# Performance work log

Measured on AMD Instinct MI355X. Metric: run time of the kernel, lower is better.

The kernel has to match this reference:

```python
import jax, jax.numpy as jnp
import numpy as np
import math

B, D, OUT = 512, 128, 100000
S, M = 32.0, 0.5
COS_M, SIN_M = math.cos(M), math.sin(M)
TH = math.cos(math.pi - M)
MM = math.sin(math.pi - M) * M
M1 = M2 = M3 = M5 = 1.0


def setup_inputs() -> dict:
    key = jax.random.key(0)
    k1, k2, k3, k4, k5, k6 = jax.random.split(key, 6)
    x = jax.random.normal(k1, (B, D), dtype=jnp.float32)
    label = jax.random.randint(k2, (B,), 0, OUT)
    k = jax.random.uniform(k3, (1, 1, 1024, 1024), dtype=jnp.float32)
    x0 = jax.random.uniform(k4, (1, 3, 112, 96), dtype=jnp.float32)
    img = jax.random.uniform(k5, (1, 3, 112, 96), dtype=jnp.float32)
    # xavier_uniform for [OUT, D]
    limit = math.sqrt(6.0 / (OUT + D))
    W = jax.random.uniform(k6, (OUT, D), minval=-limit, maxval=limit, dtype=jnp.float32)
    return {"x": x, "label": label, "k": k, "x0": x0, "img": img, "W": W}


def _arcmargin(x, W, label):
    xn = x / jnp.linalg.norm(x, axis=-1, keepdims=True)
    wn = W / jnp.linalg.norm(W, axis=-1, keepdims=True)
    cosine = xn @ wn.T                                  # [B, OUT]
    sine = jnp.sqrt(jnp.clip(1.0 - cosine * cosine, 0.0))
    phi = cosine * COS_M - sine * SIN_M
    phi = jnp.where(cosine - TH > 0, phi, cosine - MM)   # easy_margin=False
    one_hot = jax.nn.one_hot(label, OUT, dtype=cosine.dtype)
    logits = S * (one_hot * phi + (1.0 - one_hot) * cosine)
    logp = jax.nn.log_softmax(logits, axis=-1)
    return -jnp.mean(jnp.take_along_axis(logp, label[:, None], axis=1))


def _tv_loss(k):
    h, w = k.shape[-2], k.shape[-1]
    count_h = (h - 1) * w
    count_w = h * (w - 1)
    h_tv = jnp.sum((k[:, :, 1:, :] - k[:, :, :-1, :]) ** 2)
    w_tv = jnp.sum((k[:, :, :, 1:] - k[:, :, :, :-1]) ** 2)
    return -1.0 * 2.0 * (h_tv / count_h + w_tv / count_w)  # weight = -1*loss_weight


def _bin_loss(k):
    # sum over pixels of k^2 + (k-1)^2, / (h*w), then mean over batch/channel
    return jnp.mean(k * k + (k - 1.0) ** 2)


def _inv_loss(k):
    k = jax.lax.stop_gradient(k)  # original detaches before numpy FFT
    mag = jnp.abs(jnp.fft.fftn(k, axes=(-2, -1)))
    return jnp.mean(jnp.sum(mag, axis=(-1, -2)))  # L1 norm over (-1,-2), then mean


def reference(x, label, k, x0, img, W):
    loss = (M1 * _arcmargin(x, W, label)
            + M2 * _tv_loss(k)
            + M3 * _bin_loss(k)
            + M5 * _inv_loss(k))
    return loss
```

## Files before the change

kernel.cpp:

```cpp
#include <hip/hip_runtime.h>


typedef short bf16x8 __attribute__((ext_vector_type(8)));
typedef float f32x4 __attribute__((ext_vector_type(4)));
typedef unsigned short u16;
typedef unsigned int u32;

#define BATCH 512
#define DIM 128
#define OUTN 100000
#define OUTPAD 100096
#define NOBLK 782
#define CHUNKS 16
#define CHSZ 49
#define SSCALE 32.0f
#define COSM 0.8775825618903728f
#define SINM 0.479425538604203f
#define THC (-0.8775825618903728f)
#define MMC 0.2397127693021015f

#define S1_FFT 1024
#define S1_TV  2048
#define S1_XP  2176
#define S1_NW  27200

#define LDA 136

__device__ inline u16 f2bf(float f) {
  union { float f; u32 u; } v; v.f = f;
  u32 r = v.u + 0x7FFFu + ((v.u >> 16) & 1u);
  return (u16)(r >> 16);
}

__device__ inline float waveRedSum(float v) {
#pragma unroll
  for (int off = 1; off < 64; off <<= 1) v += __shfl_xor(v, off, 64);
  return v;
}

__global__ __launch_bounds__(256) void stage1_k(const float* __restrict__ x,
                                                const float* __restrict__ W,
                                                const int* __restrict__ label,
                                                const float* __restrict__ kimg,
                                                u32* __restrict__ xh,
                                                float* __restrict__ coslab,
                                                u32* __restrict__ Wh,
                                                float4* __restrict__ tvpart,
                                                float2* __restrict__ fbuf) {
  __shared__ __align__(16) float smem[2064];
  int t = threadIdx.x;
  int bid = blockIdx.x;

  if (bid < S1_FFT) {
    float* re = smem;
    float* im = smem + 1024;
    int r = bid;
#pragma unroll
    for (int i = 0; i < 4; i++) {
      int idx = i * 256 + t;
      re[idx] = kimg[r * 1024 + idx];
      im[idx] = 0.f;
    }
    __syncthreads();
    for (int lh = 9; lh >= 0; lh--) {
      int hlf = 1 << lh;
      float ang = -6.283185307179586f / (float)(hlf * 2);
#pragma unroll
      for (int i = 0; i < 2; i++) {
        int bf = i * 256 + t;
        int pos = bf & (hlf - 1);
        int g = bf >> lh;
        int i0 = (g << (lh + 1)) + pos;
        int i1 = i0 + hlf;
        float ur = re[i0], ui = im[i0], vr = re[i1], vi = im[i1];
        float s, c;
        __sincosf(ang * (float)pos, &s, &c);
        re[i0] = ur + vr; im[i0] = ui + vi;
        float dr = ur - vr, di = ui - vi;
        re[i1] = dr * c - di * s;
        im[i1] = dr * s + di * c;
      }
      __syncthreads();
    }
#pragma unroll
    for (int i = 0; i < 4; i++) {
      int idx = i * 256 + t;
      fbuf[(size_t)r * 1024 + idx] = make_float2(re[idx], im[idx]);
    }
  } else if (bid < S1_TV) {
    int r = bid - S1_FFT;
    int idx = r * 1024 + t * 4;
    float4 v = *(const float4*)&kimg[idx];
    float bs = v.x * v.x + (v.x - 1.f) * (v.x - 1.f)
             + v.y * v.y + (v.y - 1.f) * (v.y - 1.f)
             + v.z * v.z + (v.z - 1.f) * (v.z - 1.f)
             + v.w * v.w + (v.w - 1.f) * (v.w - 1.f);
    float d0 = v.y - v.x, d1 = v.z - v.y, d2 = v.w - v.z;
    float wsm = d0 * d0 + d1 * d1 + d2 * d2;
    if (t < 255) { float e4 = kimg[idx + 4]; float d3 = e4 - v.w; wsm += d3 * d3; }
    float hs = 0.f;
    if (r < 1023) {
      float4 n = *(const float4*)&kimg[idx + 1024];
      float h0 = n.x - v.x, h1 = n.y - v.y, h2 = n.z - v.z, h3 = n.w - v.w;
      hs = h0 * h0 + h1 * h1 + h2 * h2 + h3 * h3;
    }
    hs = waveRedSum(hs); wsm = waveRedSum(wsm); bs = waveRedSum(bs);
    float (*red)[4] = (float(*)[4])smem;
    if ((t & 63) == 0) { int w = t >> 6; red[0][w] = hs; red[1][w] = wsm; red[2][w] = bs; }
    __syncthreads();
    if (t == 0)
      tvpart[r] = make_float4(red[0][0] + red[0][1] + red[0][2] + red[0][3],
                              red[1][0] + red[1][1] + red[1][2] + red[1][3],
                              red[2][0] + red[2][1] + red[2][2] + red[2][3], 0.f);
  } else if (bid < S1_XP) {
    int b = (bid - S1_TV) * 4 + (t >> 6);
    int lane = t & 63;
    size_t xb = (size_t)b * DIM;
    float2 v = *(const float2*)&x[xb + lane * 2];
    int lab = label[b];
    size_t wb = (size_t)lab * DIM;
    float2 w = *(const float2*)&W[wb + lane * 2];
    float ss = waveRedSum(v.x * v.x + v.y * v.y);
    float d  = waveRedSum(v.x * w.x + v.y * w.y);
    float nw = waveRedSum(w.x * w.x + w.y * w.y);
    float inv = rsqrtf(ss);
    xh[b * 64 + lane] = (u32)f2bf(v.x * inv) | ((u32)f2bf(v.y * inv) << 16);
    if (lane == 0) coslab[b] = d * rsqrtf(ss * nw);
  } else {
    int row = (bid - S1_XP) * 4 + (t >> 6);
    int lane = t & 63;
    size_t base = (size_t)row * DIM;
    if (row < OUTN) {
      float2 v = *(const float2*)&W[base + lane * 2];
      float ss = waveRedSum(v.x * v.x + v.y * v.y);
      float inv = rsqrtf(ss);
      Wh[row * 64 + lane] = (u32)f2bf(v.x * inv) | ((u32)f2bf(v.y * inv) << 16);
    } else {
      Wh[row * 64 + lane] = 0;
    }
  }
}

__global__ __launch_bounds__(256) void stage2_k(const u16* __restrict__ Wh,
                                                const u16* __restrict__ xh,
                                                const int* __restrict__ label,
                                                float* __restrict__ gpart,
                                                const float2* __restrict__ fbuf,
                                                float* __restrict__ fftpart) {
  __shared__ __align__(16) char smem[70656];
  int t = threadIdx.x;
  int bid = blockIdx.x;

  if (bid < NOBLK) {
    u16* Ash = (u16*)smem;
    u16* Bsh = (u16*)(smem + 128 * LDA * 2);
    float* bpart = (float*)(smem + 2 * 128 * LDA * 2);
    int o0 = bid * 128;
    int wv = t >> 6, lane = t & 63;
    int wo = (wv & 1) << 6, wbs = (wv >> 1) << 6;
    int m16 = lane & 15, q = lane >> 4;
    int row = t >> 4, g = t & 15;

#pragma unroll
    for (int i = 0; i < 8; i++) {
      int f = i * 256 + t;
      int rr = f >> 4, gg = f & 15;
      *(uint4*)&Ash[rr * LDA + gg * 8] =
          *(const uint4*)&Wh[(size_t)(o0 + rr) * DIM + gg * 8];
      *(uint4*)&Bsh[rr * LDA + gg * 8] =
          *(const uint4*)&xh[(size_t)rr * DIM + gg * 8];
    }
    if (t < 128) bpart[t] = 0.f;
    __syncthreads();

    for (int bt = 0; bt < 4; bt++) {
      f32x4 acc[4][4] = {};
#pragma unroll
      for (int kk = 0; kk < 4; kk++) {
        bf16x8 af[4], bfr[4];
#pragma unroll
        for (int i = 0; i < 4; i++)
          af[i] = *(const bf16x8*)&Ash[(wo + i * 16 + m16) * LDA + kk * 32 + q * 8];
#pragma unroll
        for (int j = 0; j < 4; j++)
          bfr[j] = *(const bf16x8*)&Bsh[(wbs + j * 16 + m16) * LDA + kk * 32 + q * 8];
#pragma unroll
        for (int i = 0; i < 4; i++)
#pragma unroll
          for (int j = 0; j < 4; j++)
            acc[i][j] = __builtin_amdgcn_mfma_f32_16x16x32_bf16(af[i], bfr[j], acc[i][j], 0, 0, 0);
      }
      int b0 = bt * 128;
#pragma unroll
      for (int j = 0; j < 4; j++) {
        int b = b0 + wbs + j * 16 + m16;
        int lab = label[b];
        float s = 0.f;
#pragma unroll
        for (int i = 0; i < 4; i++) {
          int ob = o0 + wo + i * 16 + q * 4;
#pragma unroll
          for (int r = 0; r < 4; r++) {
            int o = ob + r;
            if (o < OUTN && o != lab) s += __expf(SSCALE * acc[i][j][r]);
          }
        }
        s += __shfl_xor(s, 16, 64);
        s += __shfl_xor(s, 32, 64);
        if (q == 0) atomicAdd(&bpart[wbs + j * 16 + m16], s);
      }
      __syncthreads();
      if (t < 128) gpart[(size_t)bid * 512 + b0 + t] = bpart[t];
      if (bt < 3) {
#pragma unroll
        for (int i = 0; i < 8; i++) {
          int f = i * 256 + t;
          int rr = f >> 4, gg = f & 15;
          *(uint4*)&Bsh[rr * LDA + gg * 8] =
              *(const uint4*)&xh[(size_t)((bt + 1) * 128 + rr) * DIM + gg * 8];
        }
      }
      if (t < 128) bpart[t] = 0.f;
      __syncthreads();
    }
    (void)row; (void)g;
  } else {
    float* re = (float*)smem;
    float* im = (float*)(smem + 16384);
    float* red = (float*)(smem + 32768);
    int c0 = (bid - NOBLK) * 4;
#pragma unroll
    for (int i = 0; i < 16; i++) {
      int li = i * 256 + t;
      int rr = li >> 2, c = li & 3;
      float2 v = fbuf[(size_t)rr * 1024 + c0 + c];
      re[rr * 4 + c] = v.x;
      im[rr * 4 + c] = v.y;
    }
    __syncthreads();
    for (int lh = 9; lh >= 0; lh--) {
      int hlf = 1 << lh;
      float ang = -6.283185307179586f / (float)(hlf * 2);
#pragma unroll
      for (int i = 0; i < 8; i++) {
        int w = i * 256 + t;
        int c = w & 3, bf = w >> 2;
        int pos = bf & (hlf - 1), g2i = bf >> lh;
        int i0 = ((g2i << (lh + 1)) + pos) * 4 + c;
        int i1 = i0 + hlf * 4;
        float ur = re[i0], ui = im[i0], vr = re[i1], vi = im[i1];
        float s, cc;
        __sincosf(ang * (float)pos, &s, &cc);
        re[i0] = ur + vr; im[i0] = ui + vi;
        float dr = ur - vr, di = ui - vi;
        re[i1] = dr * cc - di * s;
        im[i1] = dr * s + di * cc;
      }
      __syncthreads();
    }
    float s = 0.f;
#pragma unroll
    for (int i = 0; i < 16; i++) {
      int li = i * 256 + t;
      s += sqrtf(re[li] * re[li] + im[li] * im[li]);
    }
    s = waveRedSum(s);
    if ((t & 63) == 0) red[t >> 6] = s;
    __syncthreads();
    if (t == 0) fftpart[bid - NOBLK] = red[0] + red[1] + red[2] + red[3];
  }
}

__global__ __launch_bounds__(256) void gemmred_k(const float* __restrict__ gpart,
                                                 float* __restrict__ g2) {
  int t = threadIdx.x;
  int chunk = blockIdx.x >> 1, half = blockIdx.x & 1;
  int b = half * 256 + t;
  int oBeg = chunk * CHSZ;
  int oEnd = oBeg + CHSZ; if (oEnd > NOBLK) oEnd = NOBLK;
  float s = 0.f;
  for (int o = oBeg; o < oEnd; o++) s += gpart[(size_t)o * 512 + b];
  g2[chunk * 512 + b] = s;
}

__global__ __launch_bounds__(256) void final_k(const float* __restrict__ coslab,
                                               const float* __restrict__ g2,
                                               const float4* __restrict__ tvpart,
                                               const float* __restrict__ fftpart,
                                               float* __restrict__ out) {
  int t = threadIdx.x;
  float arc = 0.f, hs = 0.f, wsm = 0.f, bs = 0.f, fs = 0.f;
#pragma unroll
  for (int i = 0; i < 2; i++) {
    int b = i * 256 + t;
    float se = 0.f;
#pragma unroll
    for (int c = 0; c < CHUNKS; c++) se += g2[c * 512 + b];
    float cl = coslab[b];
    float sine = sqrtf(fmaxf(0.f, 1.f - cl * cl));
    float phi = cl * COSM - sine * SINM;
    if (!(cl - THC > 0.f)) phi = cl - MMC;
    arc += __logf(se + __expf(SSCALE * phi)) - SSCALE * phi;
  }
#pragma unroll
  for (int i = 0; i < 4; i++) {
    float4 p = tvpart[i * 256 + t];
    hs += p.x; wsm += p.y; bs += p.z;
  }
  fs = fftpart[t];
  arc = waveRedSum(arc); hs = waveRedSum(hs); wsm = waveRedSum(wsm);
  bs = waveRedSum(bs); fs = waveRedSum(fs);
  __shared__ float red[5][4];
  if ((t & 63) == 0) {
    int w = t >> 6;
    red[0][w] = arc; red[1][w] = hs; red[2][w] = wsm; red[3][w] = bs; red[4][w] = fs;
  }
  __syncthreads();
  if (t == 0) {
    float A = 0, H = 0, Wv = 0, Bv = 0, F = 0;
#pragma unroll
    for (int w = 0; w < 4; w++) {
      A += red[0][w]; H += red[1][w]; Wv += red[2][w]; Bv += red[3][w]; F += red[4][w];
    }
    float cnt = 1023.0f * 1024.0f;
    out[0] = A * (1.0f / 512.0f) - 2.0f * (H / cnt + Wv / cnt)
           + Bv * (1.0f / 1048576.0f) + F;
  }
}

extern "C" void kernel_launch(void* const* d_in, const int* in_sizes, int n_in,
                              void* d_out, int out_size, void* d_ws, size_t ws_size,
                              hipStream_t stream) {
  const float* x = (const float*)d_in[0];
  const int* label = (const int*)d_in[1];
  const float* kimg = (const float*)d_in[2];
  const float* W = (const float*)d_in[5];
  float* out = (float*)d_out;
  char* ws = (char*)d_ws;
  float*  coslab  = (float*)(ws + 0);
  u32*    xh      = (u32*)(ws + 2048);
  u32*    Wh      = (u32*)(ws + 133120);
  float2* fbuf    = (float2*)(ws + 25757696);
  float*  gpart   = (float*)(ws + 34146304);
  float*  g2      = (float*)(ws + 35747840);
  float4* tvpart  = (float4*)(ws + 35780608);
  float*  fftpart = (float*)(ws + 35796992);

  hipLaunchKernelGGL(stage1_k, dim3(S1_NW), dim3(256), 0, stream,
                     x, W, label, kimg, xh, coslab, Wh, tvpart, fbuf);
  hipLaunchKernelGGL(stage2_k, dim3(NOBLK + 256), dim3(256), 0, stream,
                     (const u16*)Wh, (const u16*)xh, label, gpart, fbuf, fftpart);
  hipLaunchKernelGGL(gemmred_k, dim3(CHUNKS * 2), dim3(256), 0, stream, gpart, g2);
  hipLaunchKernelGGL(final_k, dim3(1), dim3(256), 0, stream, coslab, g2, tvpart, fftpart, out);
}
```

Baseline: 165.8 us.

## Split GEMM blocks per batch tile, swizzle LDS, and correct label/padding terms afterward

The fused GEMM+logsumexp stage now launches one block per (output tile, batch tile) pair, 4x as many blocks. Each block uses a half-K double-pass with XOR-swizzled 64-wide LDS tiles instead of padded rows, which cuts shared memory enough for 4 blocks per CU. The per-element label and bounds checks are removed from the exp loop. Instead, the padded rows' constant exp(0) contribution (96) and a separately recomputed label-column exp are subtracted in the final reduction. exp is computed via exp2f with a prescaled constant, and the FFT buffer uses interleaved float2.

Result: no change. 166.3 us (+0.3%).

```diff
diff --git a/kernel.cpp b/kernel.cpp
--- a/kernel.cpp
+++ b/kernel.cpp
@@ -11,9 +11,12 @@
 #define OUTN 100000
 #define OUTPAD 100096
 #define NOBLK 782
+#define GEMMBLK 3128
+#define NROW2 1564
 #define CHUNKS 16
-#define CHSZ 49
+#define CHSZ2 98
 #define SSCALE 32.0f
+#define K2C 46.166241308446828f
 #define COSM 0.8775825618903728f
 #define SINM 0.479425538604203f
 #define THC (-0.8775825618903728f)
@@ -23,8 +26,6 @@
 #define S1_TV  2048
 #define S1_XP  2176
 #define S1_NW  27200
-
-#define LDA 136
 
 __device__ inline u16 f2bf(float f) {
   union { float f; u32 u; } v; v.f = f;
@@ -141,101 +142,81 @@
   }
 }
 
-__global__ __launch_bounds__(256) void stage2_k(const u16* __restrict__ Wh,
-                                                const u16* __restrict__ xh,
-                                                const int* __restrict__ label,
-                                                float* __restrict__ gpart,
-                                                const float2* __restrict__ fbuf,
-                                                float* __restrict__ fftpart) {
-  __shared__ __align__(16) char smem[70656];
+__global__ __launch_bounds__(256, 4) void stage2_k(const u16* __restrict__ Wh,
+                                                   const u16* __restrict__ xh,
+                                                   float* __restrict__ gpart,
+                                                   const float2* __restrict__ fbuf,
+                                                   float* __restrict__ fftpart) {
+  __shared__ __align__(16) char smem[32784];
   int t = threadIdx.x;
   int bid = blockIdx.x;
 
-  if (bid < NOBLK) {
+  if (bid < GEMMBLK) {
+    int o = bid >> 2, bt = bid & 3;
+    int o0 = o * 128, b0 = bt * 128;
     u16* Ash = (u16*)smem;
-    u16* Bsh = (u16*)(smem + 128 * LDA * 2);
-    float* bpart = (float*)(smem + 2 * 128 * LDA * 2);
-    int o0 = bid * 128;
+    u16* Bsh = (u16*)(smem + 16384);
     int wv = t >> 6, lane = t & 63;
     int wo = (wv & 1) << 6, wbs = (wv >> 1) << 6;
     int m16 = lane & 15, q = lane >> 4;
-    int row = t >> 4, g = t & 15;
-
-#pragma unroll
-    for (int i = 0; i < 8; i++) {
-      int f = i * 256 + t;
-      int rr = f >> 4, gg = f & 15;
-      *(uint4*)&Ash[rr * LDA + gg * 8] =
-          *(const uint4*)&Wh[(size_t)(o0 + rr) * DIM + gg * 8];
-      *(uint4*)&Bsh[rr * LDA + gg * 8] =
-          *(const uint4*)&xh[(size_t)rr * DIM + gg * 8];
-    }
-    if (t < 128) bpart[t] = 0.f;
-    __syncthreads();
-
-    for (int bt = 0; bt < 4; bt++) {
-      f32x4 acc[4][4] = {};
-#pragma unroll
-      for (int kk = 0; kk < 4; kk++) {
+    f32x4 acc[4][4] = {};
+
+#pragma unroll
+    for (int kc = 0; kc < 2; kc++) {
+      if (kc) __syncthreads();
+#pragma unroll
+      for (int i = 0; i < 4; i++) {
+        int f = i * 256 + t;
+        int rr = f >> 3, gg = f & 7;
+        int sw = ((gg ^ (rr & 7)) * 8);
+        *(uint4*)&Ash[rr * 64 + sw] =
+            *(const uint4*)&Wh[(size_t)(o0 + rr) * DIM + kc * 64 + gg * 8];
+        *(uint4*)&Bsh[rr * 64 + sw] =
+            *(const uint4*)&xh[(size_t)(b0 + rr) * DIM + kc * 64 + gg * 8];
+      }
+      __syncthreads();
+#pragma unroll
+      for (int kk = 0; kk < 2; kk++) {
         bf16x8 af[4], bfr[4];
 #pragma unroll
-        for (int i = 0; i < 4; i++)
-          af[i] = *(const bf16x8*)&Ash[(wo + i * 16 + m16) * LDA + kk * 32 + q * 8];
-#pragma unroll
-        for (int j = 0; j < 4; j++)
-          bfr[j] = *(const bf16x8*)&Bsh[(wbs + j * 16 + m16) * LDA + kk * 32 + q * 8];
+        for (int i = 0; i < 4; i++) {
+          int row = wo + i * 16 + m16;
+          af[i] = *(const bf16x8*)&Ash[row * 64 + (((kk * 4 + q) ^ (row & 7)) * 8)];
+        }
+#pragma unroll
+        for (int j = 0; j < 4; j++) {
+          int row = wbs + j * 16 + m16;
+          bfr[j] = *(const bf16x8*)&Bsh[row * 64 + (((kk * 4 + q) ^ (row & 7)) * 8)];
+        }
 #pragma unroll
         for (int i = 0; i < 4; i++)
 #pragma unroll
           for (int j = 0; j < 4; j++)
             acc[i][j] = __builtin_amdgcn_mfma_f32_16x16x32_bf16(af[i], bfr[j], acc[i][j], 0, 0, 0);
       }
-      int b0 = bt * 128;
-#pragma unroll
-      for (int j = 0; j < 4; j++) {
-        int b = b0 + wbs + j * 16 + m16;
-        int lab = label[b];
-        float s = 0.f;
-#pragma unroll
-        for (int i = 0; i < 4; i++) {
-          int ob = o0 + wo + i * 16 + q * 4;
-#pragma unroll
-          for (int r = 0; r < 4; r++) {
-            int o = ob + r;
-            if (o < OUTN && o != lab) s += __expf(SSCALE * acc[i][j][r]);
-          }
-        }
-        s += __shfl_xor(s, 16, 64);
-        s += __shfl_xor(s, 32, 64);
-        if (q == 0) atomicAdd(&bpart[wbs + j * 16 + m16], s);
-      }
-      __syncthreads();
-      if (t < 128) gpart[(size_t)bid * 512 + b0 + t] = bpart[t];
-      if (bt < 3) {
-#pragma unroll
-        for (int i = 0; i < 8; i++) {
-          int f = i * 256 + t;
-          int rr = f >> 4, gg = f & 15;
-          *(uint4*)&Bsh[rr * LDA + gg * 8] =
-              *(const uint4*)&xh[(size_t)((bt + 1) * 128 + rr) * DIM + gg * 8];
-        }
-      }
-      if (t < 128) bpart[t] = 0.f;
-      __syncthreads();
-    }
-    (void)row; (void)g;
+    }
+#pragma unroll
+    for (int j = 0; j < 4; j++) {
+      float s = 0.f;
+#pragma unroll
+      for (int i = 0; i < 4; i++)
+#pragma unroll
+        for (int r = 0; r < 4; r++)
+          s += exp2f(K2C * acc[i][j][r]);
+      s += __shfl_xor(s, 16, 64);
+      s += __shfl_xor(s, 32, 64);
+      if (q == 0)
+        gpart[(size_t)(o * 2 + (wv & 1)) * 512 + b0 + wbs + j * 16 + m16] = s;
+    }
   } else {
-    float* re = (float*)smem;
-    float* im = (float*)(smem + 16384);
+    float2* arr = (float2*)smem;
     float* red = (float*)(smem + 32768);
-    int c0 = (bid - NOBLK) * 4;
+    int c0 = (bid - GEMMBLK) * 4;
 #pragma unroll
     for (int i = 0; i < 16; i++) {
       int li = i * 256 + t;
       int rr = li >> 2, c = li & 3;
-      float2 v = fbuf[(size_t)rr * 1024 + c0 + c];
-      re[rr * 4 + c] = v.x;
-      im[rr * 4 + c] = v.y;
+      arr[rr * 4 + c] = fbuf[(size_t)rr * 1024 + c0 + c];
     }
     __syncthreads();
     for (int lh = 9; lh >= 0; lh--) {
@@ -248,45 +229,66 @@
         int pos = bf & (hlf - 1), g2i = bf >> lh;
         int i0 = ((g2i << (lh + 1)) + pos) * 4 + c;
         int i1 = i0 + hlf * 4;
-        float ur = re[i0], ui = im[i0], vr = re[i1], vi = im[i1];
+        float2 u = arr[i0], v = arr[i1];
         float s, cc;
         __sincosf(ang * (float)pos, &s, &cc);
-        re[i0] = ur + vr; im[i0] = ui + vi;
-        float dr = ur - vr, di = ui - vi;
-        re[i1] = dr * cc - di * s;
-        im[i1] = dr * s + di * cc;
+        arr[i0] = make_float2(u.x + v.x, u.y + v.y);
+        float dr = u.x - v.x, di = u.y - v.y;
+        arr[i1] = make_float2(dr * cc - di * s, dr * s + di * cc);
       }
       __syncthreads();
     }
     float s = 0.f;
 #pragma unroll
     for (int i = 0; i < 16; i++) {
-      int li = i * 256 + t;
-      s += sqrtf(re[li] * re[li] + im[li] * im[li]);
+      float2 v = arr[i * 256 + t];
+      s += sqrtf(v.x * v.x + v.y * v.y);
     }
     s = waveRedSum(s);
     if ((t & 63) == 0) red[t >> 6] = s;
     __syncthreads();
-    if (t == 0) fftpart[bid - NOBLK] = red[0] + red[1] + red[2] + red[3];
+    if (t == 0) fftpart[bid - GEMMBLK] = red[0] + red[1] + red[2] + red[3];
   }
 }
 
 __global__ __launch_bounds__(256) void gemmred_k(const float* __restrict__ gpart,
-                                                 float* __restrict__ g2) {
+                                                 float* __restrict__ g2,
+                                                 const u32* __restrict__ xh32,
+                                                 const u32* __restrict__ Wh32,
+                                                 const int* __restrict__ label,
+                                                 float* __restrict__ labexp) {
   int t = threadIdx.x;
-  int chunk = blockIdx.x >> 1, half = blockIdx.x & 1;
-  int b = half * 256 + t;
-  int oBeg = chunk * CHSZ;
-  int oEnd = oBeg + CHSZ; if (oEnd > NOBLK) oEnd = NOBLK;
-  float s = 0.f;
-  for (int o = oBeg; o < oEnd; o++) s += gpart[(size_t)o * 512 + b];
-  g2[chunk * 512 + b] = s;
+  int blk = blockIdx.x;
+  if (blk < 32) {
+    int chunk = blk >> 1, half = blk & 1;
+    int b = half * 256 + t;
+    int rBeg = chunk * CHSZ2;
+    int rEnd = rBeg + CHSZ2; if (rEnd > NROW2) rEnd = NROW2;
+    float s = 0.f;
+    for (int r = rBeg; r < rEnd; r++) s += gpart[(size_t)r * 512 + b];
+    g2[chunk * 512 + b] = s;
+  } else {
+    int b = (blk - 32) * 256 + t;
+    int lab = label[b];
+    const u32* xr = &xh32[b * 64];
+    const u32* wr = &Wh32[(size_t)lab * 64];
+    float d = 0.f;
+#pragma unroll 8
+    for (int i = 0; i < 64; i++) {
+      u32 xa = xr[i], wa = wr[i];
+      float xl = __uint_as_float(xa << 16), xhp = __uint_as_float(xa & 0xFFFF0000u);
+      float wl = __uint_as_float(wa << 16), whp = __uint_as_float(wa & 0xFFFF0000u);
+      d += xl * wl + xhp * whp;
+    }
+    labexp[b] = exp2f(K2C * d);
+  }
 }
 
 __global__ __launch_bounds__(256) void final_k(const float* __restrict__ coslab,
                                                const float* __restrict__ g2,
                                                const float4* __restrict__ tvpart,
                                                const float* __restrict__ fftpart,
+                                               const float* __restrict__ labexp,
                                                float* __restrict__ out) {
   int t = threadIdx.x;
   float arc = 0.f, hs = 0.f, wsm = 0.f, bs = 0.f, fs = 0.f;
@@ -296,11 +298,13 @@
     float se = 0.f;
 #pragma unroll
     for (int c = 0; c < CHUNKS; c++) se += g2[c * 512 + b];
+    se -= 96.0f;
+    se -= labexp[b];
     float cl = coslab[b];
     float sine = sqrtf(fmaxf(0.f, 1.f - cl * cl));
     float phi = cl * COSM - sine * SINM;
     if (!(cl - THC > 0.f)) phi = cl - MMC;
-    arc += __logf(se + __expf(SSCALE * phi)) - SSCALE * phi;
+    arc += __logf(se + exp2f(K2C * phi)) - SSCALE * phi;
   }
 #pragma unroll
   for (int i = 0; i < 4; i++) {
@@ -342,14 +346,17 @@
   u32*    Wh      = (u32*)(ws + 133120);
   float2* fbuf    = (float2*)(ws + 25757696);
   float*  gpart   = (float*)(ws + 34146304);
-  float*  g2      = (float*)(ws + 35747840);
-  float4* tvpart  = (float4*)(ws + 35780608);
-  float*  fftpart = (float*)(ws + 35796992);
+  float*  g2      = (float*)(ws + 35350528);
+  float4* tvpart  = (float4*)(ws + 35383296);
+  float*  fftpart = (float*)(ws + 35399680);
+  float*  labexp  = (float*)(ws + 35400704);
 
   hipLaunchKernelGGL(stage1_k, dim3(S1_NW), dim3(256), 0, stream,
                      x, W, label, kimg, xh, coslab, Wh, tvpart, fbuf);
-  hipLaunchKernelGGL(stage2_k, dim3(NOBLK + 256), dim3(256), 0, stream,
-                     (const u16*)Wh, (const u16*)xh, label, gpart, fbuf, fftpart);
-  hipLaunchKernelGGL(gemmred_k, dim3(CHUNKS * 2), dim3(256), 0, stream, gpart, g2);
-  hipLaunchKernelGGL(final_k, dim3(1), dim3(256), 0, stream, coslab, g2, tvpart, fftpart, out);
-}
+  hipLaunchKernelGGL(stage2_k, dim3(GEMMBLK + 256), dim3(256), 0, stream,
+                     (const u16*)Wh, (const u16*)xh, gpart, fbuf, fftpart);
+  hipLaunchKernelGGL(gemmred_k, dim3(34), dim3(256), 0, stream,
+                     gpart, g2, xh, Wh, label, labexp);
+  hipLaunchKernelGGL(final_k, dim3(1), dim3(256), 0, stream,
+                     coslab, g2, tvpart, fftpart, labexp, out);
+}
```
